# Optimization experiments

Hardware: AMD Instinct MI355X
Metric: run time of the kernel (lower is better)

The kernel has to match this reference:

```python
import jax, jax.numpy as jnp
import numpy as np

B, N, M, D = 64, 512, 1024, 128

def setup_inputs() -> dict:
    key = jax.random.key(0)
    ks = jax.random.split(key, 7)
    s = 1.0 / np.sqrt(D)
    return {
        "h_c": jax.random.normal(ks[0], (B, N, D), dtype=jnp.float32),
        "h_p": jax.random.normal(ks[1], (B, M, D), dtype=jnp.float32),
        "U_w": jax.random.normal(ks[2], (D, D), dtype=jnp.float32) * s,
        "U_b": jax.random.normal(ks[3], (D,), dtype=jnp.float32) * s,
        "V_w": jax.random.normal(ks[4], (D, D), dtype=jnp.float32) * s,
        "V_b": jax.random.normal(ks[5], (D,), dtype=jnp.float32) * s,
        "q": jax.random.normal(ks[6], (D,), dtype=jnp.float32),
    }

def reference(h_c, h_p, U_w, U_b, V_w, V_b, q):
    # ReLU-activated linear projections (torch Linear: x @ W.T + b)
    Uc = jax.nn.relu(jnp.einsum('bnd,ed->bne', h_c, U_w) + U_b)  # (B,N,D)
    Vp = jax.nn.relu(jnp.einsum('bmd,ed->bme', h_p, V_w) + V_b)  # (B,M,D)
    # bilinear attention scores and softmax over protein axis
    attn = jnp.einsum('bnd,bmd->bnm', Uc, Vp)                    # (B,N,M)
    weights = jax.nn.softmax(attn, axis=-1)
    context = jnp.einsum('bnm,bmd->bnd', weights, Vp)            # (B,N,D)
    joint = (Uc + context) * q                                   # (B,N,D)
    return joint.mean(axis=1)                                    # (B,D)
```

## Files before the change

### kernel.cpp

```cpp
#include <hip/hip_runtime.h>
#include <hip/hip_bf16.h>
#include <cstdint>

#define BB 64
#define NN 512
#define MM 1024
#define DD 128

typedef __bf16 bf16x8 __attribute__((ext_vector_type(8)));
typedef float f32x4 __attribute__((ext_vector_type(4)));

static __device__ __forceinline__ unsigned short f2bf(float f) {
    union { float f; unsigned int i; } v; v.f = f;
    unsigned int x = v.i;
    x += 0x7FFFu + ((x >> 16) & 1u);
    return (unsigned short)(x >> 16);
}

__global__ __launch_bounds__(256) void wconv_kernel(
    const float* __restrict__ Uw, const float* __restrict__ Vw,
    unsigned short* __restrict__ WuB, unsigned short* __restrict__ WvB,
    float* __restrict__ zbase)
{
    int tid = blockIdx.x * 256 + threadIdx.x;
    const float* src = (tid < 4096) ? Uw : Vw;
    unsigned short* dst = (tid < 4096) ? WuB : WvB;
    int idx = tid & 4095;
    float4 v = ((const float4*)src)[idx];
    ushort4 u = { f2bf(v.x), f2bf(v.y), f2bf(v.z), f2bf(v.w) };
    ((ushort4*)dst)[idx] = u;
    ((float2*)zbase)[tid] = {0.f, 0.f};
}

template<int MODE>
__global__ __launch_bounds__(256) void proj_kernel(
    const float* __restrict__ X,
    const unsigned short* __restrict__ Wbf,
    const float* __restrict__ bias,
    unsigned short* __restrict__ Y,
    unsigned short* __restrict__ YT,
    float* __restrict__ ucsum)
{
    __shared__ unsigned short Ws[128 * 136];
    __shared__ unsigned short Ts[(MODE == 1) ? 128 * 72 : 1];
    const int t = threadIdx.x;
    const int lane = t & 63;
    const int wave = t >> 6;
    const int n16 = lane & 15, q = lane >> 4;
    const long row0 = (long)blockIdx.x * 64;

    {
        const uint4* Wg = (const uint4*)Wbf;
        #pragma unroll
        for (int i = 0; i < 8; ++i) {
            int idx = i * 256 + t;
            uint4 v = Wg[idx];
            int off = idx * 8;
            *(uint4*)&Ws[(off >> 7) * 136 + (off & 127)] = v;
        }
    }
    __syncthreads();

    f32x4 acc[8];
    #pragma unroll
    for (int j = 0; j < 8; ++j) acc[j] = {0.f, 0.f, 0.f, 0.f};

    const float* xrow = X + (row0 + wave * 16 + n16) * DD + q * 8;
    #pragma unroll
    for (int kk = 0; kk < 4; ++kk) {
        float4 x0 = *(const float4*)(xrow + kk * 32);
        float4 x1 = *(const float4*)(xrow + kk * 32 + 4);
        union { bf16x8 v; unsigned short u[8]; } a;
        a.u[0] = f2bf(x0.x); a.u[1] = f2bf(x0.y); a.u[2] = f2bf(x0.z); a.u[3] = f2bf(x0.w);
        a.u[4] = f2bf(x1.x); a.u[5] = f2bf(x1.y); a.u[6] = f2bf(x1.z); a.u[7] = f2bf(x1.w);
        #pragma unroll
        for (int j = 0; j < 8; ++j) {
            bf16x8 b = *(const bf16x8*)&Ws[(j * 16 + n16) * 136 + q * 8 + kk * 32];
            acc[j] = __builtin_amdgcn_mfma_f32_16x16x32_bf16(a.v, b, acc[j], 0, 0, 0);
        }
    }

    #pragma unroll
    for (int j = 0; j < 8; ++j) {
        const int e = j * 16 + n16;
        const float bv = bias[e];
        float y[4];
        #pragma unroll
        for (int r = 0; r < 4; ++r) {
            float v = acc[j][r] + bv;
            y[r] = v > 0.f ? v : 0.f;
            Y[(row0 + wave * 16 + q * 4 + r) * DD + e] = f2bf(y[r]);
        }
        if (MODE == 1) {
            ushort4 u = { f2bf(y[0]), f2bf(y[1]), f2bf(y[2]), f2bf(y[3]) };
            *(ushort4*)&Ts[e * 72 + wave * 16 + q * 4] = u;
        } else {
            float s = (y[0] + y[1]) + (y[2] + y[3]);
            s += __shfl_xor(s, 16);
            s += __shfl_xor(s, 32);
            if (q == 0) {
                const long b = row0 >> 9;
                atomicAdd(&ucsum[b * DD + e], s);
            }
        }
    }

    if (MODE == 1) {
        __syncthreads();
        const long b = row0 >> 10;
        const long mt = (row0 & 1023) >> 6;
        unsigned short* dst = YT + ((b * 16 + mt) * 128) * 64;
        #pragma unroll
        for (int i = 0; i < 4; ++i) {
            int idx = i * 256 + t;
            int e = idx >> 3, m = (idx & 7) * 8;
            uint4 v = *(const uint4*)&Ts[e * 72 + m];
            ((uint4*)dst)[idx] = v;
        }
    }
}

__global__ __launch_bounds__(256) void attn_kernel(
    const unsigned short* __restrict__ Uc,
    const unsigned short* __restrict__ Vp,
    const unsigned short* __restrict__ VpT,
    float* __restrict__ ctx)
{
    __shared__ unsigned short Vs[64 * 136];
    __shared__ unsigned short VTs[128 * 72];
    __shared__ unsigned short Ps[4][16 * 72];

    const int t = threadIdx.x;
    const int lane = t & 63;
    const int wave = t >> 6;
    const int n16 = lane & 15, q = lane >> 4;

    const int id = blockIdx.x;
    const int xcd = id & 7;
    const int slot = id >> 3;
    const int b = xcd * 8 + (slot >> 3);
    const int nt = slot & 7;

    const unsigned short* ucb = Uc + ((long)b * NN + nt * 64 + wave * 16) * DD;
    const unsigned short* vpb = Vp + (long)b * MM * DD;
    const unsigned short* vtb = VpT + (long)b * 16 * DD * 64;

    bf16x8 Bg[4];
    #pragma unroll
    for (int kk = 0; kk < 4; ++kk)
        Bg[kk] = *(const bf16x8*)&ucb[n16 * DD + q * 8 + kk * 32];

    f32x4 O[8];
    #pragma unroll
    for (int j = 0; j < 8; ++j) O[j] = {0.f, 0.f, 0.f, 0.f};
    float lpart = 0.f;
    const float LOG2E = 1.44269504088896f;

    for (int mt = 0; mt < 16; ++mt) {
        __syncthreads();
        {
            const uint4* s1 = (const uint4*)(vpb + mt * 64 * DD);
            const uint4* s2 = (const uint4*)(vtb + mt * DD * 64);
            #pragma unroll
            for (int i = 0; i < 4; ++i) {
                int idx = i * 256 + t;
                uint4 v1 = s1[idx];
                uint4 v2 = s2[idx];
                int off = idx * 8;
                *(uint4*)&Vs[(off >> 7) * 136 + (off & 127)] = v1;
                *(uint4*)&VTs[(off >> 6) * 72 + (off & 63)] = v2;
            }
        }
        __syncthreads();

        f32x4 S[4];
        #pragma unroll
        for (int j = 0; j < 4; ++j) S[j] = {0.f, 0.f, 0.f, 0.f};
        #pragma unroll
        for (int kk = 0; kk < 4; ++kk) {
            #pragma unroll
            for (int j = 0; j < 4; ++j) {
                bf16x8 a = *(const bf16x8*)&Vs[(j * 16 + n16) * 136 + q * 8 + kk * 32];
                S[j] = __builtin_amdgcn_mfma_f32_16x16x32_bf16(a, Bg[kk], S[j], 0, 0, 0);
            }
        }

        #pragma unroll
        for (int j = 0; j < 4; ++j) {
            float p0 = __builtin_exp2f(S[j][0] * LOG2E);
            float p1 = __builtin_exp2f(S[j][1] * LOG2E);
            float p2 = __builtin_exp2f(S[j][2] * LOG2E);
            float p3 = __builtin_exp2f(S[j][3] * LOG2E);
            lpart += (p0 + p1) + (p2 + p3);
            ushort4 u = { f2bf(p0), f2bf(p1), f2bf(p2), f2bf(p3) };
            *(ushort4*)&Ps[wave][n16 * 72 + j * 16 + q * 4] = u;
        }

        #pragma unroll
        for (int kk = 0; kk < 2; ++kk) {
            bf16x8 a = *(const bf16x8*)&Ps[wave][n16 * 72 + kk * 32 + q * 8];
            #pragma unroll
            for (int j = 0; j < 8; ++j) {
                bf16x8 bb = *(const bf16x8*)&VTs[(j * 16 + n16) * 72 + kk * 32 + q * 8];
                O[j] = __builtin_amdgcn_mfma_f32_16x16x32_bf16(a, bb, O[j], 0, 0, 0);
            }
        }
    }

    lpart += __shfl_xor(lpart, 16);
    lpart += __shfl_xor(lpart, 32);

    float inv[4];
    #pragma unroll
    for (int r = 0; r < 4; ++r)
        inv[r] = 1.0f / __shfl(lpart, q * 4 + r);
    #pragma unroll
    for (int j = 0; j < 8; ++j) {
        float s = O[j][0] * inv[0] + O[j][1] * inv[1]
                + O[j][2] * inv[2] + O[j][3] * inv[3];
        s += __shfl_xor(s, 16);
        s += __shfl_xor(s, 32);
        if (q == 0)
            atomicAdd(&ctx[b * DD + j * 16 + n16], s);
    }
}

__global__ __launch_bounds__(256) void finalize_kernel(
    const float* __restrict__ ctx, const float* __restrict__ ucsum,
    const float* __restrict__ qv, float* __restrict__ out)
{
    int i = blockIdx.x * 256 + threadIdx.x;
    int d = i & 127;
    out[i] = (ctx[i] + ucsum[i]) * qv[d] * (1.0f / (float)NN);
}

extern "C" void kernel_launch(void* const* d_in, const int* in_sizes, int n_in,
                              void* d_out, int out_size, void* d_ws, size_t ws_size,
                              hipStream_t stream) {
    const float* h_c = (const float*)d_in[0];
    const float* h_p = (const float*)d_in[1];
    const float* U_w = (const float*)d_in[2];
    const float* U_b = (const float*)d_in[3];
    const float* V_w = (const float*)d_in[4];
    const float* V_b = (const float*)d_in[5];
    const float* qv  = (const float*)d_in[6];
    float* out = (float*)d_out;

    unsigned short* Uc  = (unsigned short*)d_ws;
    unsigned short* Vp  = Uc  + (size_t)BB * NN * DD;
    unsigned short* VpT = Vp  + (size_t)BB * MM * DD;
    unsigned short* WuB = VpT + (size_t)BB * DD * MM;
    unsigned short* WvB = WuB + (size_t)DD * DD;
    float* ctx   = (float*)(WvB + (size_t)DD * DD);
    float* ucsum = ctx + (size_t)BB * DD;

    wconv_kernel<<<32, 256, 0, stream>>>(U_w, V_w, WuB, WvB, ctx);
    proj_kernel<0><<<BB * NN / 64, 256, 0, stream>>>(h_c, WuB, U_b, Uc, nullptr, ucsum);
    proj_kernel<1><<<BB * MM / 64, 256, 0, stream>>>(h_p, WvB, V_b, Vp, VpT, nullptr);
    attn_kernel<<<512, 256, 0, stream>>>(Uc, Vp, VpT, ctx);
    finalize_kernel<<<BB * DD / 256, 256, 0, stream>>>(ctx, ucsum, qv, out);
}
```

Measured before the change: 155.5 us.

## Fuse Uc projection into attention kernel and register-prefetch Vp tiles

Computes the h_c projection (Uc) inside the attention kernel instead of a separate launch, so Uc is never written to or read from global memory. The Uc column sum is folded into the context atomic. The attention loop now prefetches the next Vp/VpT tile into registers while the current tile is in LDS. The V projection stages its outputs in LDS so global stores are coalesced, and bf16 conversion uses paired intrinsics. The cost is more LDS and registers in the attention kernel, which may lower occupancy.

```diff
diff --git a/kernel.cpp b/kernel.cpp
--- a/kernel.cpp
+++ b/kernel.cpp
@@ -16,33 +16,37 @@
     x += 0x7FFFu + ((x >> 16) & 1u);
     return (unsigned short)(x >> 16);
 }
+static __device__ __forceinline__ unsigned int f2bf2(float a, float b) {
+    union { __hip_bfloat162 h; unsigned int u; } c;
+    c.h = __float22bfloat162_rn(make_float2(a, b));
+    return c.u;
+}
 
 __global__ __launch_bounds__(256) void wconv_kernel(
     const float* __restrict__ Uw, const float* __restrict__ Vw,
     unsigned short* __restrict__ WuB, unsigned short* __restrict__ WvB,
-    float* __restrict__ zbase)
+    float* __restrict__ ctx)
 {
     int tid = blockIdx.x * 256 + threadIdx.x;
     const float* src = (tid < 4096) ? Uw : Vw;
     unsigned short* dst = (tid < 4096) ? WuB : WvB;
     int idx = tid & 4095;
     float4 v = ((const float4*)src)[idx];
-    ushort4 u = { f2bf(v.x), f2bf(v.y), f2bf(v.z), f2bf(v.w) };
-    ((ushort4*)dst)[idx] = u;
-    ((float2*)zbase)[tid] = {0.f, 0.f};
-}
-
-template<int MODE>
-__global__ __launch_bounds__(256) void proj_kernel(
+    uint2 u = { f2bf2(v.x, v.y), f2bf2(v.z, v.w) };
+    ((uint2*)dst)[idx] = u;
+    if (tid < 4096) ((float2*)ctx)[tid] = {0.f, 0.f};
+}
+
+__global__ __launch_bounds__(256) void proj_v_kernel(
     const float* __restrict__ X,
     const unsigned short* __restrict__ Wbf,
     const float* __restrict__ bias,
     unsigned short* __restrict__ Y,
-    unsigned short* __restrict__ YT,
-    float* __restrict__ ucsum)
+    unsigned short* __restrict__ YT)
 {
-    __shared__ unsigned short Ws[128 * 136];
-    __shared__ unsigned short Ts[(MODE == 1) ? 128 * 72 : 1];
+    __shared__ __align__(16) unsigned short Ws[128 * 136];
+    unsigned short* Ys = Ws;
+    unsigned short* Ts = Ws + 8192;
     const int t = threadIdx.x;
     const int lane = t & 63;
     const int wave = t >> 6;
@@ -70,9 +74,9 @@
     for (int kk = 0; kk < 4; ++kk) {
         float4 x0 = *(const float4*)(xrow + kk * 32);
         float4 x1 = *(const float4*)(xrow + kk * 32 + 4);
-        union { bf16x8 v; unsigned short u[8]; } a;
-        a.u[0] = f2bf(x0.x); a.u[1] = f2bf(x0.y); a.u[2] = f2bf(x0.z); a.u[3] = f2bf(x0.w);
-        a.u[4] = f2bf(x1.x); a.u[5] = f2bf(x1.y); a.u[6] = f2bf(x1.z); a.u[7] = f2bf(x1.w);
+        union { bf16x8 v; unsigned int u[4]; } a;
+        a.u[0] = f2bf2(x0.x, x0.y); a.u[1] = f2bf2(x0.z, x0.w);
+        a.u[2] = f2bf2(x1.x, x1.y); a.u[3] = f2bf2(x1.z, x1.w);
         #pragma unroll
         for (int j = 0; j < 8; ++j) {
             bf16x8 b = *(const bf16x8*)&Ws[(j * 16 + n16) * 136 + q * 8 + kk * 32];
@@ -80,55 +84,60 @@
         }
     }
 
+    unsigned short yb[8][4];
     #pragma unroll
     for (int j = 0; j < 8; ++j) {
-        const int e = j * 16 + n16;
-        const float bv = bias[e];
+        const float bv = bias[j * 16 + n16];
         float y[4];
         #pragma unroll
         for (int r = 0; r < 4; ++r) {
             float v = acc[j][r] + bv;
             y[r] = v > 0.f ? v : 0.f;
-            Y[(row0 + wave * 16 + q * 4 + r) * DD + e] = f2bf(y[r]);
-        }
-        if (MODE == 1) {
-            ushort4 u = { f2bf(y[0]), f2bf(y[1]), f2bf(y[2]), f2bf(y[3]) };
-            *(ushort4*)&Ts[e * 72 + wave * 16 + q * 4] = u;
-        } else {
-            float s = (y[0] + y[1]) + (y[2] + y[3]);
-            s += __shfl_xor(s, 16);
-            s += __shfl_xor(s, 32);
-            if (q == 0) {
-                const long b = row0 >> 9;
-                atomicAdd(&ucsum[b * DD + e], s);
-            }
-        }
-    }
-
-    if (MODE == 1) {
-        __syncthreads();
+        }
+        uint2 u = { f2bf2(y[0], y[1]), f2bf2(y[2], y[3]) };
+        *(uint2*)&yb[j][0] = u;
+    }
+    __syncthreads();
+
+    #pragma unroll
+    for (int j = 0; j < 8; ++j) {
+        const int e = j * 16 + n16;
+        #pragma unroll
+        for (int r = 0; r < 4; ++r)
+            Ys[(wave * 16 + q * 4 + r) * 128 + e] = yb[j][r];
+        *(uint2*)&Ts[e * 72 + wave * 16 + q * 4] = *(uint2*)&yb[j][0];
+    }
+    __syncthreads();
+
+    {
+        uint4* dstY = (uint4*)(Y + row0 * DD);
         const long b = row0 >> 10;
         const long mt = (row0 & 1023) >> 6;
-        unsigned short* dst = YT + ((b * 16 + mt) * 128) * 64;
+        uint4* dstT = (uint4*)(YT + ((b * 16 + mt) * 128) * 64);
         #pragma unroll
         for (int i = 0; i < 4; ++i) {
             int idx = i * 256 + t;
+            dstY[idx] = ((const uint4*)Ys)[idx];
             int e = idx >> 3, m = (idx & 7) * 8;
-            uint4 v = *(const uint4*)&Ts[e * 72 + m];
-            ((uint4*)dst)[idx] = v;
+            dstT[idx] = *(const uint4*)&Ts[e * 72 + m];
         }
     }
 }
 
 __global__ __launch_bounds__(256) void attn_kernel(
-    const unsigned short* __restrict__ Uc,
+    const float* __restrict__ hc,
+    const unsigned short* __restrict__ WuB,
+    const float* __restrict__ Ub,
     const unsigned short* __restrict__ Vp,
     const unsigned short* __restrict__ VpT,
     float* __restrict__ ctx)
 {
-    __shared__ unsigned short Vs[64 * 136];
-    __shared__ unsigned short VTs[128 * 72];
-    __shared__ unsigned short Ps[4][16 * 72];
+    __shared__ __align__(16) unsigned char smem[52224];
+    unsigned short* Ws  = (unsigned short*)smem;
+    unsigned short* Ucs = Ws + 128 * 136;
+    unsigned short* Vs  = (unsigned short*)smem;
+    unsigned short* VTs = Vs + 64 * 136;
+    unsigned short* Ps  = VTs + 128 * 72;
 
     const int t = threadIdx.x;
     const int lane = t & 63;
@@ -141,14 +150,68 @@
     const int b = xcd * 8 + (slot >> 3);
     const int nt = slot & 7;
 
-    const unsigned short* ucb = Uc + ((long)b * NN + nt * 64 + wave * 16) * DD;
     const unsigned short* vpb = Vp + (long)b * MM * DD;
     const unsigned short* vtb = VpT + (long)b * 16 * DD * 64;
 
+    {
+        const uint4* Wg = (const uint4*)WuB;
+        #pragma unroll
+        for (int i = 0; i < 8; ++i) {
+            int idx = i * 256 + t;
+            uint4 v = Wg[idx];
+            int off = idx * 8;
+            *(uint4*)&Ws[(off >> 7) * 136 + (off & 127)] = v;
+        }
+    }
+    __syncthreads();
+
+    f32x4 acc[8];
+    #pragma unroll
+    for (int j = 0; j < 8; ++j) acc[j] = {0.f, 0.f, 0.f, 0.f};
+    {
+        const float* xrow = hc + ((long)b * NN + nt * 64 + wave * 16 + n16) * DD + q * 8;
+        #pragma unroll
+        for (int kk = 0; kk < 4; ++kk) {
+            float4 x0 = *(const float4*)(xrow + kk * 32);
+            float4 x1 = *(const float4*)(xrow + kk * 32 + 4);
+            union { bf16x8 v; unsigned int u[4]; } a;
+            a.u[0] = f2bf2(x0.x, x0.y); a.u[1] = f2bf2(x0.z, x0.w);
+            a.u[2] = f2bf2(x1.x, x1.y); a.u[3] = f2bf2(x1.z, x1.w);
+            #pragma unroll
+            for (int j = 0; j < 8; ++j) {
+                bf16x8 bb = *(const bf16x8*)&Ws[(j * 16 + n16) * 136 + q * 8 + kk * 32];
+                acc[j] = __builtin_amdgcn_mfma_f32_16x16x32_bf16(a.v, bb, acc[j], 0, 0, 0);
+            }
+        }
+    }
+    float ucred[8];
+    #pragma unroll
+    for (int j = 0; j < 8; ++j) {
+        const float bv = Ub[j * 16 + n16];
+        float s = 0.f;
+        #pragma unroll
+        for (int r = 0; r < 4; ++r) {
+            float v = acc[j][r] + bv;
+            v = v > 0.f ? v : 0.f;
+            s += v;
+            Ucs[(wave * 16 + q * 4 + r) * 136 + j * 16 + n16] = f2bf(v);
+        }
+        ucred[j] = s;
+    }
+    __syncthreads();
+
     bf16x8 Bg[4];
     #pragma unroll
     for (int kk = 0; kk < 4; ++kk)
-        Bg[kk] = *(const bf16x8*)&ucb[n16 * DD + q * 8 + kk * 32];
+        Bg[kk] = *(const bf16x8*)&Ucs[(wave * 16 + n16) * 136 + q * 8 + kk * 32];
+
+    uint4 pa[4], pb[4];
+    #pragma unroll
+    for (int i = 0; i < 4; ++i) {
+        pa[i] = ((const uint4*)(vpb))[i * 256 + t];
+        pb[i] = ((const uint4*)(vtb))[i * 256 + t];
+    }
+    __syncthreads();
 
     f32x4 O[8];
     #pragma unroll
@@ -157,18 +220,20 @@
     const float LOG2E = 1.44269504088896f;
 
     for (int mt = 0; mt < 16; ++mt) {
-        __syncthreads();
-        {
-            const uint4* s1 = (const uint4*)(vpb + mt * 64 * DD);
-            const uint4* s2 = (const uint4*)(vtb + mt * DD * 64);
+        #pragma unroll
+        for (int i = 0; i < 4; ++i) {
+            int idx = i * 256 + t;
+            int off = idx * 8;
+            *(uint4*)&Vs[(off >> 7) * 136 + (off & 127)] = pa[i];
+            *(uint4*)&VTs[(off >> 6) * 72 + (off & 63)] = pb[i];
+        }
+        if (mt < 15) {
+            const uint4* s1 = (const uint4*)(vpb + (mt + 1) * 64 * DD);
+            const uint4* s2 = (const uint4*)(vtb + (mt + 1) * DD * 64);
             #pragma unroll
             for (int i = 0; i < 4; ++i) {
-                int idx = i * 256 + t;
-                uint4 v1 = s1[idx];
-                uint4 v2 = s2[idx];
-                int off = idx * 8;
-                *(uint4*)&Vs[(off >> 7) * 136 + (off & 127)] = v1;
-                *(uint4*)&VTs[(off >> 6) * 72 + (off & 63)] = v2;
+                pa[i] = s1[i * 256 + t];
+                pb[i] = s2[i * 256 + t];
             }
         }
         __syncthreads();
@@ -192,19 +257,20 @@
             float p2 = __builtin_exp2f(S[j][2] * LOG2E);
             float p3 = __builtin_exp2f(S[j][3] * LOG2E);
             lpart += (p0 + p1) + (p2 + p3);
-            ushort4 u = { f2bf(p0), f2bf(p1), f2bf(p2), f2bf(p3) };
-            *(ushort4*)&Ps[wave][n16 * 72 + j * 16 + q * 4] = u;
+            uint2 u = { f2bf2(p0, p1), f2bf2(p2, p3) };
+            *(uint2*)&Ps[wave * (16 * 72) + n16 * 72 + j * 16 + q * 4] = u;
         }
 
         #pragma unroll
         for (int kk = 0; kk < 2; ++kk) {
-            bf16x8 a = *(const bf16x8*)&Ps[wave][n16 * 72 + kk * 32 + q * 8];
+            bf16x8 a = *(const bf16x8*)&Ps[wave * (16 * 72) + n16 * 72 + kk * 32 + q * 8];
             #pragma unroll
             for (int j = 0; j < 8; ++j) {
                 bf16x8 bb = *(const bf16x8*)&VTs[(j * 16 + n16) * 72 + kk * 32 + q * 8];
                 O[j] = __builtin_amdgcn_mfma_f32_16x16x32_bf16(a, bb, O[j], 0, 0, 0);
             }
         }
+        __syncthreads();
     }
 
     lpart += __shfl_xor(lpart, 16);
@@ -216,7 +282,8 @@
         inv[r] = 1.0f / __shfl(lpart, q * 4 + r);
     #pragma unroll
     for (int j = 0; j < 8; ++j) {
-        float s = O[j][0] * inv[0] + O[j][1] * inv[1]
+        float s = ucred[j]
+                + O[j][0] * inv[0] + O[j][1] * inv[1]
                 + O[j][2] * inv[2] + O[j][3] * inv[3];
         s += __shfl_xor(s, 16);
         s += __shfl_xor(s, 32);
@@ -226,12 +293,11 @@
 }
 
 __global__ __launch_bounds__(256) void finalize_kernel(
-    const float* __restrict__ ctx, const float* __restrict__ ucsum,
-    const float* __restrict__ qv, float* __restrict__ out)
+    const float* __restrict__ ctx, const float* __restrict__ qv,
+    float* __restrict__ out)
 {
     int i = blockIdx.x * 256 + threadIdx.x;
-    int d = i & 127;
-    out[i] = (ctx[i] + ucsum[i]) * qv[d] * (1.0f / (float)NN);
+    out[i] = ctx[i] * qv[i & 127] * (1.0f / (float)NN);
 }
 
 extern "C" void kernel_launch(void* const* d_in, const int* in_sizes, int n_in,
@@ -246,17 +312,14 @@
     const float* qv  = (const float*)d_in[6];
     float* out = (float*)d_out;
 
-    unsigned short* Uc  = (unsigned short*)d_ws;
-    unsigned short* Vp  = Uc  + (size_t)BB * NN * DD;
+    unsigned short* Vp  = (unsigned short*)d_ws;
     unsigned short* VpT = Vp  + (size_t)BB * MM * DD;
     unsigned short* WuB = VpT + (size_t)BB * DD * MM;
     unsigned short* WvB = WuB + (size_t)DD * DD;
-    float* ctx   = (float*)(WvB + (size_t)DD * DD);
-    float* ucsum = ctx + (size_t)BB * DD;
+    float* ctx = (float*)(WvB + (size_t)DD * DD);
 
     wconv_kernel<<<32, 256, 0, stream>>>(U_w, V_w, WuB, WvB, ctx);
-    proj_kernel<0><<<BB * NN / 64, 256, 0, stream>>>(h_c, WuB, U_b, Uc, nullptr, ucsum);
-    proj_kernel<1><<<BB * MM / 64, 256, 0, stream>>>(h_p, WvB, V_b, Vp, VpT, nullptr);
-    attn_kernel<<<512, 256, 0, stream>>>(Uc, Vp, VpT, ctx);
-    finalize_kernel<<<BB * DD / 256, 256, 0, stream>>>(ctx, ucsum, qv, out);
-}
+    proj_v_kernel<<<BB * MM / 64, 256, 0, stream>>>(h_p, WvB, V_b, Vp, VpT);
+    attn_kernel<<<512, 256, 0, stream>>>(h_c, WuB, U_b, Vp, VpT, ctx);
+    finalize_kernel<<<BB * DD / 256, 256, 0, stream>>>(ctx, qv, out);
+}
```

Result: slower. 200.4 us (+28.8%).
